# Kernel tuning notes

Hardware: AMD Instinct MI355X
Metric: run time of the kernel (lower is better)

Reference implementation:

```python
import jax, jax.numpy as jnp
import numpy as np

N_STEPS = 256          # ray-marching samples per ray
DENSITY_SCALE = 10.0   # sigma scale (extinction coefficient multiplier)
EPS = 1e-8


def _trilerp(grid, x, y, z):
    """Trilinear interpolation. grid: [D,H,W]; x,y,z: voxel coords ([...])."""
    D, H, W = grid.shape
    x0 = jnp.clip(jnp.floor(x), 0, W - 2).astype(jnp.int32)
    y0 = jnp.clip(jnp.floor(y), 0, H - 2).astype(jnp.int32)
    z0 = jnp.clip(jnp.floor(z), 0, D - 2).astype(jnp.int32)
    fx = jnp.clip(x - x0, 0.0, 1.0)
    fy = jnp.clip(y - y0, 0.0, 1.0)
    fz = jnp.clip(z - z0, 0.0, 1.0)
    x1, y1, z1 = x0 + 1, y0 + 1, z0 + 1
    c000 = grid[z0, y0, x0]; c001 = grid[z0, y0, x1]
    c010 = grid[z0, y1, x0]; c011 = grid[z0, y1, x1]
    c100 = grid[z1, y0, x0]; c101 = grid[z1, y0, x1]
    c110 = grid[z1, y1, x0]; c111 = grid[z1, y1, x1]
    c00 = c000 * (1 - fx) + c001 * fx
    c01 = c010 * (1 - fx) + c011 * fx
    c10 = c100 * (1 - fx) + c101 * fx
    c11 = c110 * (1 - fx) + c111 * fx
    c0 = c00 * (1 - fy) + c01 * fy
    c1 = c10 * (1 - fy) + c11 * fy
    return c0 * (1 - fz) + c1 * fz


def _transmittance(rays, grid):
    """rays: [N,6] (origin, direction); grid: [D,H,W] clamped densities in [0,1].
    Marches through the [-1,1]^3 box and returns per-ray transmittance [N]."""
    D, H, W = grid.shape
    o = rays[:, 0:3]                                  # [N,3]
    d = rays[:, 3:6]
    d = d / (jnp.linalg.norm(d, axis=-1, keepdims=True) + EPS)
    # ray-box intersection with the unit box [-1,1]^3 (safe reciprocal)
    inv_d = 1.0 / jnp.where(jnp.abs(d) < EPS, jnp.sign(d) * EPS + EPS, d)
    t_a = (-1.0 - o) * inv_d
    t_b = (1.0 - o) * inv_d
    tmin = jnp.max(jnp.minimum(t_a, t_b), axis=-1)    # [N]
    tmax = jnp.min(jnp.maximum(t_a, t_b), axis=-1)
    tmin = jnp.maximum(tmin, 0.0)
    valid = tmax > tmin
    seg = jnp.where(valid, tmax - tmin, 0.0)          # traversed length
    # midpoint sample positions along each ray: [N, S, 3]
    frac = (jnp.arange(N_STEPS, dtype=grid.dtype) + 0.5) / N_STEPS
    ts = tmin[:, None] + seg[:, None] * frac[None, :]          # [N,S]
    pos = o[:, None, :] + ts[:, :, None] * d[:, None, :]        # [N,S,3]
    # map [-1,1] -> voxel coordinates
    gx = (pos[..., 0] + 1.0) * 0.5 * (W - 1)
    gy = (pos[..., 1] + 1.0) * 0.5 * (H - 1)
    gz = (pos[..., 2] + 1.0) * 0.5 * (D - 1)
    sigma = _trilerp(grid, gx, gy, gz)                 # [N,S]
    dt = seg / N_STEPS                                 # [N]
    tau = DENSITY_SCALE * jnp.sum(sigma, axis=-1) * dt
    return jnp.where(valid, jnp.exp(-tau), 1.0)


def setup_inputs() -> dict:
    key = jax.random.key(0)
    k_rays, k_grid = jax.random.split(key)
    rays = jax.random.normal(k_rays, (65536, 6), dtype=jnp.float32)
    grid = jax.random.uniform(k_grid, (256, 256, 256), dtype=jnp.float32)
    return {"rays": rays, "Grid": grid}


def reference(rays, Grid):
    # TrainableCloud.forward: renderer(rays, clamp(Grid, 0, 1))
    return _transmittance(rays, jnp.clip(Grid, 0.0, 1.0))
```

## Files before the change

kernel.cpp:

```cpp
#include <hip/hip_runtime.h>
#include <hip/hip_fp16.h>
#include <math.h>
#include <stdint.h>

#define N_STEPS 256
#define DENSITY_SCALE 10.0f
#define REF_EPS 1e-8f

typedef uint32_t u32_a2 __attribute__((aligned(2)));
typedef uint2 uint2_a4 __attribute__((aligned(4)));

__device__ __forceinline__ float clip01(float v) {
    return fminf(fmaxf(v, 0.0f), 1.0f);
}

__device__ __forceinline__ float safe_inv(float d) {
    float denom = d;
    if (fabsf(d) < REF_EPS) {
        float s = (d > 0.0f) ? 1.0f : ((d < 0.0f) ? -1.0f : 0.0f);
        denom = s * REF_EPS + REF_EPS;
    }
    return 1.0f / denom;
}

__device__ __forceinline__ uint32_t q255(float v) {
    return (uint32_t)__float2int_rn(clip01(v) * 255.0f);
}

__global__ __launch_bounds__(256) void repack_quad_kernel(
    const float* __restrict__ g, uint32_t* __restrict__ quad, int* __restrict__ counter)
{
    if (blockIdx.x == 0 && threadIdx.x == 0) *counter = 0;
    int t = blockIdx.x * blockDim.x + threadIdx.x;
    int x4 = (t & 63) << 2;
    int zy = t >> 6;
    int z = zy >> 8;
    int y = zy & 255;
    int yp = (y == 255) ? y : y + 1;
    int zp = (z == 255) ? z : z + 1;
    float4 a = *(const float4*)(g + ((z  << 16) + (y  << 8) + x4));
    float4 b = *(const float4*)(g + ((z  << 16) + (yp << 8) + x4));
    float4 c = *(const float4*)(g + ((zp << 16) + (y  << 8) + x4));
    float4 d = *(const float4*)(g + ((zp << 16) + (yp << 8) + x4));
    uint4 o;
    o.x = q255(a.x) | (q255(b.x) << 8) | (q255(c.x) << 16) | (q255(d.x) << 24);
    o.y = q255(a.y) | (q255(b.y) << 8) | (q255(c.y) << 16) | (q255(d.y) << 24);
    o.z = q255(a.z) | (q255(b.z) << 8) | (q255(c.z) << 16) | (q255(d.z) << 24);
    o.w = q255(a.w) | (q255(b.w) << 8) | (q255(c.w) << 16) | (q255(d.w) << 24);
    *(uint4*)(quad + ((zy << 8) + x4)) = o;
}

__global__ __launch_bounds__(256) void setup_kernel(
    const float* __restrict__ rays, float* __restrict__ out,
    float* __restrict__ compactF, int* __restrict__ compactI,
    int* __restrict__ counter, int n_rays)
{
    int ray = blockIdx.x * blockDim.x + threadIdx.x;
    bool valid = false;
    float ox = 0, oy = 0, oz = 0, dx = 0, dy = 0, dz = 0, tmin = 0, seg = 0;

    if (ray < n_rays) {
        const float* r = rays + ray * 6;
        ox = r[0]; oy = r[1]; oz = r[2];
        dx = r[3]; dy = r[4]; dz = r[5];
        float nrm = sqrtf(dx*dx + dy*dy + dz*dz) + REF_EPS;
        float inv_n = 1.0f / nrm;
        dx *= inv_n; dy *= inv_n; dz *= inv_n;
        float ixv = safe_inv(dx), iyv = safe_inv(dy), izv = safe_inv(dz);
        float tax = (-1.0f - ox) * ixv, tbx = (1.0f - ox) * ixv;
        float tay = (-1.0f - oy) * iyv, tby = (1.0f - oy) * iyv;
        float taz = (-1.0f - oz) * izv, tbz = (1.0f - oz) * izv;
        tmin = fmaxf(fmaxf(fminf(tax, tbx), fminf(tay, tby)), fminf(taz, tbz));
        float tmax = fminf(fminf(fmaxf(tax, tbx), fmaxf(tay, tby)), fmaxf(taz, tbz));
        tmin = fmaxf(tmin, 0.0f);
        valid = tmax > tmin;
        seg = valid ? (tmax - tmin) : 0.0f;
    }

    unsigned long long mask = __ballot(valid);
    int lane = threadIdx.x & 63;
    int nbefore = __popcll(mask & ((1ull << lane) - 1ull));
    int total = __popcll(mask);
    int base = 0;
    if (lane == 0) base = atomicAdd(counter, total);
    base = __shfl(base, 0);

    if (valid) {
        int idx = base + nbefore;
        float4* dst = (float4*)(compactF + (size_t)idx * 8);
        dst[0] = make_float4(ox, oy, oz, dx);
        dst[1] = make_float4(dy, dz, tmin, seg);
        compactI[idx] = ray;
    } else if (ray < n_rays) {
        out[ray] = 1.0f;
    }
}

__global__ __launch_bounds__(256, 8) void march_kernel(
    const float* __restrict__ compactF, const int* __restrict__ compactI,
    const int* __restrict__ counter, const uint32_t* __restrict__ quad,
    float* __restrict__ out)
{
    int gid = blockIdx.x * blockDim.x + threadIdx.x;
    int sub = gid & 15;
    int nvalid = *counter;
    int stride = (gridDim.x * blockDim.x) >> 4;

    for (int ray = gid >> 4; ray < nvalid; ray += stride) {
        const float4* c = (const float4*)(compactF + (size_t)ray * 8);
        float4 c0 = c[0], c1 = c[1];
        float ox = c0.x, oy = c0.y, oz = c0.z;
        float dx = c0.w, dy = c1.x, dz = c1.y;
        float tmin = c1.z, seg = c1.w;

        float s   = seg * (1.0f / (float)N_STEPS);
        float t0  = fmaf(0.5f, s, tmin);
        float dxs = dx * 127.5f, dys = dy * 127.5f, dzs = dz * 127.5f;
        float gsx = dxs * s, gsy = dys * s, gsz = dzs * s;
        float gx0 = fmaf(t0, dxs, fmaf(ox, 127.5f, 127.5f));
        float gy0 = fmaf(t0, dys, fmaf(oy, 127.5f, 127.5f));
        float gz0 = fmaf(t0, dzs, fmaf(oz, 127.5f, 127.5f));

        float sum = 0.0f;
        #pragma unroll 8
        for (int i = sub; i < N_STEPS; i += 16) {
            float fi = (float)i;
            float gx = fmaf(fi, gsx, gx0);
            float gy = fmaf(fi, gsy, gy0);
            float gz = fmaf(fi, gsz, gz0);

            float fx0 = floorf(gx), fy0 = floorf(gy), fz0 = floorf(gz);
            int x0 = (int)fminf(fmaxf(fx0, 0.0f), 254.0f);
            int y0 = (int)fminf(fmaxf(fy0, 0.0f), 254.0f);
            int z0 = (int)fminf(fmaxf(fz0, 0.0f), 254.0f);
            float fx = fminf(fmaxf(gx - (float)x0, 0.0f), 1.0f);
            float fy = fminf(fmaxf(gy - (float)y0, 0.0f), 1.0f);
            float fz = fminf(fmaxf(gz - (float)z0, 0.0f), 1.0f);

            int vidx = (z0 << 16) + (y0 << 8) + x0;
            uint2 v = *(const uint2_a4*)(quad + vidx);
            float c000 = (float)( v.x        & 0xffu);
            float c010 = (float)((v.x >>  8) & 0xffu);
            float c100 = (float)((v.x >> 16) & 0xffu);
            float c110 = (float)( v.x >> 24        );
            float c001 = (float)( v.y        & 0xffu);
            float c011 = (float)((v.y >>  8) & 0xffu);
            float c101 = (float)((v.y >> 16) & 0xffu);
            float c111 = (float)( v.y >> 24        );

            float omfx = 1.0f - fx;
            float c00 = c000 * omfx + c001 * fx;
            float c01 = c010 * omfx + c011 * fx;
            float c10 = c100 * omfx + c101 * fx;
            float c11 = c110 * omfx + c111 * fx;
            float omfy = 1.0f - fy;
            float cc0 = c00 * omfy + c01 * fy;
            float cc1 = c10 * omfy + c11 * fy;
            sum += cc0 * (1.0f - fz) + cc1 * fz;
        }

        sum += __shfl_xor(sum, 1);
        sum += __shfl_xor(sum, 2);
        sum += __shfl_xor(sum, 4);
        sum += __shfl_xor(sum, 8);

        if (sub == 0) {
            float dt = seg * (1.0f / (float)N_STEPS);
            float tau = (DENSITY_SCALE / 255.0f) * sum * dt;
            out[compactI[ray]] = expf(-tau);
        }
    }
}

__global__ __launch_bounds__(256) void repack_kernel(
    const float* __restrict__ g, __half* __restrict__ gh, int n)
{
    int i = (blockIdx.x * blockDim.x + threadIdx.x) * 4;
    if (i >= n) return;
    float4 v = *(const float4*)(g + i);
    __half2* dst = (__half2*)(gh + i);
    dst[0] = __floats2half2_rn(clip01(v.x), clip01(v.y));
    dst[1] = __floats2half2_rn(clip01(v.z), clip01(v.w));
}

__global__ __launch_bounds__(256) void transmittance_h_kernel(
    const float* __restrict__ rays, const __half* __restrict__ gh,
    float* __restrict__ out, int n_rays)
{
    int gid = blockIdx.x * blockDim.x + threadIdx.x;
    int ray = gid >> 3;
    int sub = gid & 7;
    if (ray >= n_rays) return;

    const float* r = rays + ray * 6;
    float ox = r[0], oy = r[1], oz = r[2];
    float dx = r[3], dy = r[4], dz = r[5];
    float nrm = sqrtf(dx*dx + dy*dy + dz*dz) + REF_EPS;
    float inv_n = 1.0f / nrm;
    dx *= inv_n; dy *= inv_n; dz *= inv_n;
    float ixv = safe_inv(dx), iyv = safe_inv(dy), izv = safe_inv(dz);
    float tax = (-1.0f - ox) * ixv, tbx = (1.0f - ox) * ixv;
    float tay = (-1.0f - oy) * iyv, tby = (1.0f - oy) * iyv;
    float taz = (-1.0f - oz) * izv, tbz = (1.0f - oz) * izv;
    float tmin = fmaxf(fmaxf(fminf(tax, tbx), fminf(tay, tby)), fminf(taz, tbz));
    float tmax = fminf(fminf(fmaxf(tax, tbx), fmaxf(tay, tby)), fmaxf(taz, tbz));
    tmin = fmaxf(tmin, 0.0f);
    bool valid = tmax > tmin;
    float seg = valid ? (tmax - tmin) : 0.0f;
    float sum = 0.0f;

    if (valid) {
        #pragma unroll 4
        for (int i = sub; i < N_STEPS; i += 8) {
            float frac = ((float)i + 0.5f) * (1.0f / (float)N_STEPS);
            float t = fmaf(seg, frac, tmin);
            float px = fmaf(t, dx, ox);
            float py = fmaf(t, dy, oy);
            float pz = fmaf(t, dz, oz);
            float gx = (px + 1.0f) * (0.5f * 255.0f);
            float gy = (py + 1.0f) * (0.5f * 255.0f);
            float gz = (pz + 1.0f) * (0.5f * 255.0f);
            float fx0 = floorf(gx), fy0 = floorf(gy), fz0 = floorf(gz);
            int x0 = (int)fminf(fmaxf(fx0, 0.0f), 254.0f);
            int y0 = (int)fminf(fmaxf(fy0, 0.0f), 254.0f);
            int z0 = (int)fminf(fmaxf(fz0, 0.0f), 254.0f);
            float fx = fminf(fmaxf(gx - (float)x0, 0.0f), 1.0f);
            float fy = fminf(fmaxf(gy - (float)y0, 0.0f), 1.0f);
            float fz = fminf(fmaxf(gz - (float)z0, 0.0f), 1.0f);
            const __half* p0 = gh + ((z0 << 16) + (y0 << 8) + x0);
            u32_a2 a00 = *(const u32_a2*)(const void*)(p0);
            u32_a2 a01 = *(const u32_a2*)(const void*)(p0 + 256);
            u32_a2 a10 = *(const u32_a2*)(const void*)(p0 + 65536);
            u32_a2 a11 = *(const u32_a2*)(const void*)(p0 + 65536 + 256);
            float2 f00 = __half22float2(*(__half2*)&a00);
            float2 f01 = __half22float2(*(__half2*)&a01);
            float2 f10 = __half22float2(*(__half2*)&a10);
            float2 f11 = __half22float2(*(__half2*)&a11);
            float omfx = 1.0f - fx;
            float c00 = f00.x * omfx + f00.y * fx;
            float c01 = f01.x * omfx + f01.y * fx;
            float c10 = f10.x * omfx + f10.y * fx;
            float c11 = f11.x * omfx + f11.y * fx;
            float omfy = 1.0f - fy;
            float cc0 = c00 * omfy + c01 * fy;
            float cc1 = c10 * omfy + c11 * fy;
            sum += cc0 * (1.0f - fz) + cc1 * fz;
        }
    }

    sum += __shfl_xor(sum, 1);
    sum += __shfl_xor(sum, 2);
    sum += __shfl_xor(sum, 4);

    if (sub == 0) {
        float result = 1.0f;
        if (valid) {
            float dt = seg * (1.0f / (float)N_STEPS);
            float tau = DENSITY_SCALE * sum * dt;
            result = expf(-tau);
        }
        out[ray] = result;
    }
}

__global__ __launch_bounds__(256) void transmittance_kernel(
    const float* __restrict__ rays, const float* __restrict__ grid,
    float* __restrict__ out, int n_rays)
{
    int gid = blockIdx.x * blockDim.x + threadIdx.x;
    int ray = gid >> 2;
    int sub = gid & 3;
    if (ray >= n_rays) return;
    const float* r = rays + ray * 6;
    float ox = r[0], oy = r[1], oz = r[2];
    float dx = r[3], dy = r[4], dz = r[5];
    float nrm = sqrtf(dx*dx + dy*dy + dz*dz) + REF_EPS;
    float inv_n = 1.0f / nrm;
    dx *= inv_n; dy *= inv_n; dz *= inv_n;
    float ixv = safe_inv(dx), iyv = safe_inv(dy), izv = safe_inv(dz);
    float tax = (-1.0f - ox) * ixv, tbx = (1.0f - ox) * ixv;
    float tay = (-1.0f - oy) * iyv, tby = (1.0f - oy) * iyv;
    float taz = (-1.0f - oz) * izv, tbz = (1.0f - oz) * izv;
    float tmin = fmaxf(fmaxf(fminf(tax, tbx), fminf(tay, tby)), fminf(taz, tbz));
    float tmax = fminf(fminf(fmaxf(tax, tbx), fmaxf(tay, tby)), fmaxf(taz, tbz));
    tmin = fmaxf(tmin, 0.0f);
    bool valid = tmax > tmin;
    float result = 1.0f;
    float seg = valid ? (tmax - tmin) : 0.0f;
    float sum = 0.0f;
    if (valid) {
        #pragma unroll 4
        for (int i = sub; i < N_STEPS; i += 4) {
            float frac = ((float)i + 0.5f) * (1.0f / (float)N_STEPS);
            float t = fmaf(seg, frac, tmin);
            float px = fmaf(t, dx, ox);
            float py = fmaf(t, dy, oy);
            float pz = fmaf(t, dz, oz);
            float gx = (px + 1.0f) * (0.5f * 255.0f);
            float gy = (py + 1.0f) * (0.5f * 255.0f);
            float gz = (pz + 1.0f) * (0.5f * 255.0f);
            float fx0 = floorf(gx), fy0 = floorf(gy), fz0 = floorf(gz);
            int x0 = (int)fminf(fmaxf(fx0, 0.0f), 254.0f);
            int y0 = (int)fminf(fmaxf(fy0, 0.0f), 254.0f);
            int z0 = (int)fminf(fmaxf(fz0, 0.0f), 254.0f);
            float fx = fminf(fmaxf(gx - (float)x0, 0.0f), 1.0f);
            float fy = fminf(fmaxf(gy - (float)y0, 0.0f), 1.0f);
            float fz = fminf(fmaxf(gz - (float)z0, 0.0f), 1.0f);
            const float* p0 = grid + ((z0 << 16) + (y0 << 8) + x0);
            const float* p1 = p0 + 65536;
            float c000 = p0[0],   c001 = p0[1];
            float c010 = p0[256], c011 = p0[257];
            float c100 = p1[0],   c101 = p1[1];
            float c110 = p1[256], c111 = p1[257];
            float omfx = 1.0f - fx;
            float c00 = c000 * omfx + c001 * fx;
            float c01 = c010 * omfx + c011 * fx;
            float c10 = c100 * omfx + c101 * fx;
            float c11 = c110 * omfx + c111 * fx;
            float omfy = 1.0f - fy;
            float cc0 = c00 * omfy + c01 * fy;
            float cc1 = c10 * omfy + c11 * fy;
            sum += cc0 * (1.0f - fz) + cc1 * fz;
        }
    }
    sum += __shfl_xor(sum, 1);
    sum += __shfl_xor(sum, 2);
    if (valid) {
        float dt = seg * (1.0f / (float)N_STEPS);
        float tau = DENSITY_SCALE * sum * dt;
        result = expf(-tau);
    }
    if (sub == 0) out[ray] = result;
}

extern "C" void kernel_launch(void* const* d_in, const int* in_sizes, int n_in,
                              void* d_out, int out_size, void* d_ws, size_t ws_size,
                              hipStream_t stream) {
    const float* rays = (const float*)d_in[0];
    const float* grid = (const float*)d_in[1];
    float* out = (float*)d_out;
    int n_rays = in_sizes[0] / 6;
    int n_grid = in_sizes[1];

    const size_t QUAD_BYTES = (size_t)n_grid * 4;
    const size_t CF_BYTES   = (size_t)n_rays * 8 * 4;
    const size_t CI_BYTES   = (size_t)n_rays * 4;
    const size_t need_full  = QUAD_BYTES + CF_BYTES + CI_BYTES + 256;
    const size_t need_half  = (size_t)n_grid * 2;

    if (ws_size >= need_full) {
        uint32_t* quad    = (uint32_t*)d_ws;
        float*    compactF = (float*)((char*)d_ws + QUAD_BYTES);
        int*      compactI = (int*)((char*)d_ws + QUAD_BYTES + CF_BYTES);
        int*      counter  = (int*)((char*)d_ws + QUAD_BYTES + CF_BYTES + CI_BYTES);

        int rp_threads = n_grid / 4;
        repack_quad_kernel<<<(rp_threads + 255) / 256, 256, 0, stream>>>(grid, quad, counter);
        setup_kernel<<<(n_rays + 255) / 256, 256, 0, stream>>>(
            rays, out, compactF, compactI, counter, n_rays);
        march_kernel<<<4096, 256, 0, stream>>>(compactF, compactI, counter, quad, out);
    } else if (ws_size >= need_half) {
        __half* gh = (__half*)d_ws;
        int rp_threads = n_grid / 4;
        repack_kernel<<<(rp_threads + 255) / 256, 256, 0, stream>>>(grid, gh, n_grid);
        int total_threads = n_rays * 8;
        transmittance_h_kernel<<<(total_threads + 255) / 256, 256, 0, stream>>>(
            rays, gh, out, n_rays);
    } else {
        int total_threads = n_rays * 4;
        transmittance_kernel<<<(total_threads + 255) / 256, 256, 0, stream>>>(
            rays, grid, out, n_rays);
    }
}
```

Before: 180.8 us.

## Fuse ray setup into march kernel and drop valid-ray compaction

Merges the setup kernel into the march kernel so each 16-lane group computes the ray-box intersection itself and writes 1.0 for rays that miss the box. This removes one kernel launch, the atomic compaction pass and the round trip of compacted ray data through global memory. In exchange, invalid rays now occupy grid-stride loop slots, so work is less evenly balanced than with the dense compacted list, and every lane recomputes the intersection.

```diff
diff --git a/kernel.cpp b/kernel.cpp
--- a/kernel.cpp
+++ b/kernel.cpp
@@ -28,9 +28,8 @@
 }
 
 __global__ __launch_bounds__(256) void repack_quad_kernel(
-    const float* __restrict__ g, uint32_t* __restrict__ quad, int* __restrict__ counter)
-{
-    if (blockIdx.x == 0 && threadIdx.x == 0) *counter = 0;
+    const float* __restrict__ g, uint32_t* __restrict__ quad)
+{
     int t = blockIdx.x * blockDim.x + threadIdx.x;
     int x4 = (t & 63) << 2;
     int zy = t >> 6;
@@ -50,19 +49,18 @@
     *(uint4*)(quad + ((zy << 8) + x4)) = o;
 }
 
-__global__ __launch_bounds__(256) void setup_kernel(
-    const float* __restrict__ rays, float* __restrict__ out,
-    float* __restrict__ compactF, int* __restrict__ compactI,
-    int* __restrict__ counter, int n_rays)
-{
-    int ray = blockIdx.x * blockDim.x + threadIdx.x;
-    bool valid = false;
-    float ox = 0, oy = 0, oz = 0, dx = 0, dy = 0, dz = 0, tmin = 0, seg = 0;
-
-    if (ray < n_rays) {
+__global__ __launch_bounds__(256, 8) void march_all_kernel(
+    const float* __restrict__ rays, const uint32_t* __restrict__ quad,
+    float* __restrict__ out, int n_rays)
+{
+    int gid = blockIdx.x * blockDim.x + threadIdx.x;
+    int sub = gid & 15;
+    int stride = (gridDim.x * blockDim.x) >> 4;
+
+    for (int ray = gid >> 4; ray < n_rays; ray += stride) {
         const float* r = rays + ray * 6;
-        ox = r[0]; oy = r[1]; oz = r[2];
-        dx = r[3]; dy = r[4]; dz = r[5];
+        float ox = r[0], oy = r[1], oz = r[2];
+        float dx = r[3], dy = r[4], dz = r[5];
         float nrm = sqrtf(dx*dx + dy*dy + dz*dz) + REF_EPS;
         float inv_n = 1.0f / nrm;
         dx *= inv_n; dy *= inv_n; dz *= inv_n;
@@ -70,48 +68,14 @@
         float tax = (-1.0f - ox) * ixv, tbx = (1.0f - ox) * ixv;
         float tay = (-1.0f - oy) * iyv, tby = (1.0f - oy) * iyv;
         float taz = (-1.0f - oz) * izv, tbz = (1.0f - oz) * izv;
-        tmin = fmaxf(fmaxf(fminf(tax, tbx), fminf(tay, tby)), fminf(taz, tbz));
+        float tmin = fmaxf(fmaxf(fminf(tax, tbx), fminf(tay, tby)), fminf(taz, tbz));
         float tmax = fminf(fminf(fmaxf(tax, tbx), fmaxf(tay, tby)), fmaxf(taz, tbz));
         tmin = fmaxf(tmin, 0.0f);
-        valid = tmax > tmin;
-        seg = valid ? (tmax - tmin) : 0.0f;
-    }
-
-    unsigned long long mask = __ballot(valid);
-    int lane = threadIdx.x & 63;
-    int nbefore = __popcll(mask & ((1ull << lane) - 1ull));
-    int total = __popcll(mask);
-    int base = 0;
-    if (lane == 0) base = atomicAdd(counter, total);
-    base = __shfl(base, 0);
-
-    if (valid) {
-        int idx = base + nbefore;
-        float4* dst = (float4*)(compactF + (size_t)idx * 8);
-        dst[0] = make_float4(ox, oy, oz, dx);
-        dst[1] = make_float4(dy, dz, tmin, seg);
-        compactI[idx] = ray;
-    } else if (ray < n_rays) {
-        out[ray] = 1.0f;
-    }
-}
-
-__global__ __launch_bounds__(256, 8) void march_kernel(
-    const float* __restrict__ compactF, const int* __restrict__ compactI,
-    const int* __restrict__ counter, const uint32_t* __restrict__ quad,
-    float* __restrict__ out)
-{
-    int gid = blockIdx.x * blockDim.x + threadIdx.x;
-    int sub = gid & 15;
-    int nvalid = *counter;
-    int stride = (gridDim.x * blockDim.x) >> 4;
-
-    for (int ray = gid >> 4; ray < nvalid; ray += stride) {
-        const float4* c = (const float4*)(compactF + (size_t)ray * 8);
-        float4 c0 = c[0], c1 = c[1];
-        float ox = c0.x, oy = c0.y, oz = c0.z;
-        float dx = c0.w, dy = c1.x, dz = c1.y;
-        float tmin = c1.z, seg = c1.w;
+        if (!(tmax > tmin)) {
+            if (sub == 0) out[ray] = 1.0f;
+            continue;
+        }
+        float seg = tmax - tmin;
 
         float s   = seg * (1.0f / (float)N_STEPS);
         float t0  = fmaf(0.5f, s, tmin);
@@ -167,7 +131,7 @@
         if (sub == 0) {
             float dt = seg * (1.0f / (float)N_STEPS);
             float tau = (DENSITY_SCALE / 255.0f) * sum * dt;
-            out[compactI[ray]] = expf(-tau);
+            out[ray] = expf(-tau);
         }
     }
 }
@@ -343,22 +307,13 @@
     int n_grid = in_sizes[1];
 
     const size_t QUAD_BYTES = (size_t)n_grid * 4;
-    const size_t CF_BYTES   = (size_t)n_rays * 8 * 4;
-    const size_t CI_BYTES   = (size_t)n_rays * 4;
-    const size_t need_full  = QUAD_BYTES + CF_BYTES + CI_BYTES + 256;
     const size_t need_half  = (size_t)n_grid * 2;
 
-    if (ws_size >= need_full) {
-        uint32_t* quad    = (uint32_t*)d_ws;
-        float*    compactF = (float*)((char*)d_ws + QUAD_BYTES);
-        int*      compactI = (int*)((char*)d_ws + QUAD_BYTES + CF_BYTES);
-        int*      counter  = (int*)((char*)d_ws + QUAD_BYTES + CF_BYTES + CI_BYTES);
-
+    if (ws_size >= QUAD_BYTES) {
+        uint32_t* quad = (uint32_t*)d_ws;
         int rp_threads = n_grid / 4;
-        repack_quad_kernel<<<(rp_threads + 255) / 256, 256, 0, stream>>>(grid, quad, counter);
-        setup_kernel<<<(n_rays + 255) / 256, 256, 0, stream>>>(
-            rays, out, compactF, compactI, counter, n_rays);
-        march_kernel<<<4096, 256, 0, stream>>>(compactF, compactI, counter, quad, out);
+        repack_quad_kernel<<<(rp_threads + 255) / 256, 256, 0, stream>>>(grid, quad);
+        march_all_kernel<<<4096, 256, 0, stream>>>(rays, quad, out, n_rays);
     } else if (ws_size >= need_half) {
         __half* gh = (__half*)d_ws;
         int rp_threads = n_grid / 4;
```

After: 161.7 us. 10.5% less time.
